# Optimization experiments

Hardware: AMD Instinct MI355X
Metric: run time of the kernel (lower is better)

## Reference

```python
import jax, jax.numpy as jnp
import numpy as np

B, T, V, D, DH, H = 4, 512, 32000, 768, 768, 4  # batch, seq, vocab, dim_in, dim_out(per-head & ffn), heads


def layer_norm(x, g, b, eps=1e-5):
    m = jnp.mean(x, axis=-1, keepdims=True)
    v = jnp.mean((x - m) ** 2, axis=-1, keepdims=True)
    return (x - m) * jax.lax.rsqrt(v + eps) * g + b


def setup_inputs() -> dict:
    key = jax.random.key(0)
    ks = jax.random.split(key, 20)
    s = 0.02
    f = lambda k, shp: (jax.random.normal(k, shp, jnp.float32) * s)
    return {
        "x": jax.random.randint(ks[0], (B, T), 0, V),
        "attention_mask": jax.random.randint(ks[1], (B, 1, T), 0, 2).astype(bool),
        "token_embed": f(ks[2], (V, D)),
        "segment_embed": f(ks[3], (V, D)),
        "ln_embed_g": jnp.ones((D,), jnp.float32), "ln_embed_b": jnp.zeros((D,), jnp.float32),
        "Wq": f(ks[4], (H, D, DH)), "bq": f(ks[5], (H, DH)),
        "Wk": f(ks[6], (H, D, DH)), "bk": f(ks[7], (H, DH)),
        "Wv": f(ks[8], (H, D, DH)), "bv": f(ks[9], (H, DH)),
        "Wo": f(ks[10], (H * DH, D)), "bo": f(ks[11], (D,)),
        "ln_attn_g": jnp.ones((D,), jnp.float32), "ln_attn_b": jnp.zeros((D,), jnp.float32),
        "W1": f(ks[12], (D, DH)), "b1": f(ks[13], (DH,)),
        "W2": f(ks[14], (DH, D)), "b2": f(ks[15], (D,)),
        "ln_enc_g": jnp.ones((D,), jnp.float32), "ln_enc_b": jnp.zeros((D,), jnp.float32),
        "Wproj": f(ks[16], (D, V)), "bproj": f(ks[17], (V,)),
        "Wcls": f(ks[18], (D, 2)), "bcls": f(ks[19], (2,)),
    }


def reference(x, attention_mask, token_embed, segment_embed, ln_embed_g, ln_embed_b,
              Wq, bq, Wk, bk, Wv, bv, Wo, bo, ln_attn_g, ln_attn_b,
              W1, b1, W2, b2, ln_enc_g, ln_enc_b, Wproj, bproj, Wcls, bcls):
    Bsz, Tlen = x.shape
    dim = token_embed.shape[1]
    # JointEmbedding: segment tensor is 0 for first half, 1 afterwards
    seg = jnp.zeros_like(x).at[:, Tlen // 2 + 1:].set(1)
    # positional encoding (faithful to source: exponent is 2*j/dim per column j,
    # sin on even columns, cos on odd columns, applied to pos/10000**exp)
    d = 2.0 * jnp.arange(dim, dtype=jnp.float32) / dim            # [D]
    p = jnp.arange(Tlen, dtype=jnp.float32)[:, None] / (10000.0 ** d)  # [T, D]
    pe = jnp.where(jnp.arange(dim) % 2 == 0, jnp.sin(p), jnp.cos(p))   # [T, D]
    emb = token_embed[x] + segment_embed[seg] + pe[None]          # [B, T, D]
    emb = layer_norm(emb, ln_embed_g, ln_embed_b)

    # Multi-head attention (vectorized over the per-head Python loop)
    Q = jnp.einsum('btd,hde->bhte', emb, Wq) + bq[None, :, None, :]
    K = jnp.einsum('btd,hde->bhte', emb, Wk) + bk[None, :, None, :]
    Vh = jnp.einsum('btd,hde->bhte', emb, Wv) + bv[None, :, None, :]
    # NOTE: source scales by seq_len**-0.5 (Q.size(1)), not head_dim**-0.5
    scores = jnp.einsum('bhte,bhse->bhts', Q, K) * (float(Tlen) ** -0.5)
    # NOTE: source masked_fill_'s with value 1e-9 (not -inf) before softmax
    scores = jnp.where(attention_mask[:, None, :, :], 1e-9, scores)
    attn = jax.nn.softmax(scores, axis=-1)
    ctx = jnp.einsum('bhts,bhse->bhte', attn, Vh)                 # [B, H, T, DH]
    cat = ctx.transpose(0, 2, 1, 3).reshape(Bsz, Tlen, -1)        # head concat order
    attn_out = layer_norm(cat @ Wo + bo, ln_attn_g, ln_attn_b)

    # FFN (no residual in source; dropout is identity at inference)
    h = jax.nn.gelu(attn_out @ W1 + b1, approximate=False)
    enc = layer_norm(h @ W2 + b2, ln_enc_g, ln_enc_b)

    token_pred = enc @ Wproj + bproj                              # [B, T, V]
    logits = jax.nn.log_softmax(token_pred, axis=-1)
    cls_out = enc[:, 0, :] @ Wcls + bcls                          # [B, 2]
    return logits, cls_out
```

## Files before the change

kernel.cpp:

```cpp
#include <hip/hip_runtime.h>
#include <hip/hip_bf16.h>
#include <stdint.h>

#define B_ 4
#define T_ 512
#define V_ 32000
#define D_ 768
#define DH_ 768
#define H_ 4
#define R_ 2048

typedef unsigned short u16;
typedef __attribute__((ext_vector_type(4))) float f32x4;
typedef __attribute__((ext_vector_type(8))) short s16x8;
typedef __attribute__((ext_vector_type(8))) unsigned short u16x8;
typedef __attribute__((address_space(3))) char* lds_cp;
typedef const __attribute__((address_space(1))) char* gl_cp;

__device__ __forceinline__ float bf2f(u16 u){
  union { float f; unsigned int i; } w; w.i = ((unsigned int)u) << 16; return w.f;
}
__device__ __forceinline__ u16 f2bf(float f){
  union { float f; unsigned int i; } w; w.f = f;
  unsigned int r = w.i + 0x7fffu + ((w.i >> 16) & 1u);
  return (u16)(r >> 16);
}

__device__ __forceinline__ float block_sum(float v, float* red){
  #pragma unroll
  for (int o = 32; o; o >>= 1) v += __shfl_down(v, o);
  __syncthreads();
  if ((threadIdx.x & 63) == 0) red[threadIdx.x >> 6] = v;
  __syncthreads();
  return red[0] + red[1] + red[2] + red[3];
}
__device__ __forceinline__ float block_max(float v, float* red){
  #pragma unroll
  for (int o = 32; o; o >>= 1) v = fmaxf(v, __shfl_down(v, o));
  __syncthreads();
  if ((threadIdx.x & 63) == 0) red[threadIdx.x >> 6] = v;
  __syncthreads();
  return fmaxf(fmaxf(red[0], red[1]), fmaxf(red[2], red[3]));
}

__global__ void mask_convert(const void* __restrict__ mraw, int* __restrict__ mout){
  __shared__ int isbyte;
  if (threadIdx.x == 0) isbyte = 0;
  __syncthreads();
  const unsigned char* by = (const unsigned char*)mraw;
  int f = 0;
  for (int i = threadIdx.x; i < 2048; i += 256)
    if ((i & 3) && by[i]) f = 1;
  if (f) atomicOr(&isbyte, 1);
  __syncthreads();
  if (isbyte){
    for (int i = threadIdx.x; i < 2048; i += 256) mout[i] = by[i] ? 1 : 0;
  } else {
    const int* mi = (const int*)mraw;
    for (int i = threadIdx.x; i < 2048; i += 256) mout[i] = mi[i] ? 1 : 0;
  }
}

__global__ __launch_bounds__(256)
void transpose_all(const float* __restrict__ Wq, const float* __restrict__ Wk,
                   const float* __restrict__ Wv, const float* __restrict__ Wo,
                   const float* __restrict__ W1, const float* __restrict__ W2,
                   u16* __restrict__ wqT, u16* __restrict__ wkT,
                   u16* __restrict__ wvT, u16* __restrict__ woT,
                   u16* __restrict__ w1T, u16* __restrict__ w2T){
  __shared__ u16 tile[32][33];
  int z = blockIdx.z;
  const float* in; u16* out; int out_ld = 768;
  if (z < 4)      { in = Wq + (long)z * 589824;        out = wqT + (long)z * 589824; }
  else if (z < 8) { int k = z - 4;  in = Wk + (long)k * 589824; out = wkT + (long)k * 589824; }
  else if (z < 12){ int k = z - 8;  in = Wv + (long)k * 589824; out = wvT + (long)k * 589824; }
  else if (z < 16){ int k = z - 12; in = Wo + (long)k * 589824; out = woT + (long)k * 768; out_ld = 3072; }
  else if (z == 16){ in = W1; out = w1T; }
  else             { in = W2; out = w2T; }
  int c0 = blockIdx.x * 32, r0 = blockIdx.y * 32;
  int tx = threadIdx.x & 31, ty = threadIdx.x >> 5;
  #pragma unroll
  for (int i = 0; i < 32; i += 8)
    tile[ty + i][tx] = f2bf(in[(long)(r0 + ty + i) * 768 + (c0 + tx)]);
  __syncthreads();
  #pragma unroll
  for (int i = 0; i < 32; i += 8)
    out[(long)(c0 + ty + i) * out_ld + (r0 + tx)] = tile[tx][ty + i];
}

__global__ __launch_bounds__(256)
void transpose_f2b(const float* __restrict__ in, u16* __restrict__ out, int R, int C){
  __shared__ u16 tile[32][33];
  int c0 = blockIdx.x * 32, r0 = blockIdx.y * 32;
  int tx = threadIdx.x & 31, ty = threadIdx.x >> 5;
  #pragma unroll
  for (int i = 0; i < 32; i += 8)
    tile[ty + i][tx] = f2bf(in[(long)(r0 + ty + i) * C + (c0 + tx)]);
  __syncthreads();
  #pragma unroll
  for (int i = 0; i < 32; i += 8)
    out[(long)(c0 + ty + i) * R + (r0 + tx)] = tile[tx][ty + i];
}

__global__ __launch_bounds__(256)
void embed_ln(const int* __restrict__ x, const float* __restrict__ tok,
              const float* __restrict__ seg, const float* __restrict__ g,
              const float* __restrict__ bb, u16* __restrict__ emb){
  __shared__ float red[4];
  int r = blockIdx.x, t = r & 511;
  int tid = threadIdx.x;
  long trow = (long)x[r] * D_;
  long srow = (t > 256) ? (long)D_ : 0;
  float v[3];
  float s = 0.f;
  #pragma unroll
  for (int q = 0; q < 3; ++q){
    int j = tid + q * 256;
    float d = (2.0f * (float)j) * (1.0f / 768.0f);
    float p = (float)t * powf(10000.0f, -d);
    float pe = (j & 1) ? cosf(p) : sinf(p);
    v[q] = tok[trow + j] + seg[srow + j] + pe;
    s += v[q];
  }
  float mean = block_sum(s, red) * (1.0f / 768.0f);
  float vs = 0.f;
  #pragma unroll
  for (int q = 0; q < 3; ++q){ float dd = v[q] - mean; vs += dd * dd; }
  float var = block_sum(vs, red) * (1.0f / 768.0f);
  float inv = rsqrtf(var + 1e-5f);
  #pragma unroll
  for (int q = 0; q < 3; ++q){
    int j = tid + q * 256;
    emb[(long)r * D_ + j] = f2bf((v[q] - mean) * inv * g[j] + bb[j]);
  }
}

__global__ __launch_bounds__(256)
void ln_rows(const u16* __restrict__ in, const float* __restrict__ g,
             const float* __restrict__ bb, u16* __restrict__ out){
  __shared__ float red[4];
  long r = blockIdx.x;
  int tid = threadIdx.x;
  const u16* row = in + r * D_;
  float v[3];
  float s = 0.f;
  #pragma unroll
  for (int q = 0; q < 3; ++q){ v[q] = bf2f(row[tid + q * 256]); s += v[q]; }
  float mean = block_sum(s, red) * (1.0f / 768.0f);
  float vs = 0.f;
  #pragma unroll
  for (int q = 0; q < 3; ++q){ float dd = v[q] - mean; vs += dd * dd; }
  float var = block_sum(vs, red) * (1.0f / 768.0f);
  float inv = rsqrtf(var + 1e-5f);
  #pragma unroll
  for (int q = 0; q < 3; ++q){
    int j = tid + q * 256;
    out[r * D_ + j] = f2bf((v[q] - mean) * inv * g[j] + bb[j]);
  }
}

__global__ __launch_bounds__(256)
void attn_softmax(u16* __restrict__ S, const int* __restrict__ mask){
  __shared__ float red[4];
  int t = blockIdx.x, z = blockIdx.y, b = z >> 2;
  u16* row = S + (long)z * (T_ * T_) + (long)t * T_;
  int tid = threadIdx.x;
  int s0 = tid, s1 = tid + 256;
  float v0 = mask[b * T_ + s0] ? 1e-9f : bf2f(row[s0]);
  float v1 = mask[b * T_ + s1] ? 1e-9f : bf2f(row[s1]);
  float mx = block_max(fmaxf(v0, v1), red);
  float e0 = expf(v0 - mx), e1 = expf(v1 - mx);
  float l = block_sum(e0 + e1, red);
  float inv = 1.0f / l;
  row[s0] = f2bf(e0 * inv);
  row[s1] = f2bf(e1 * inv);
}

__global__ __launch_bounds__(256)
void lsm_b2f(const u16* __restrict__ pred, float* __restrict__ out){
  __shared__ float sm[256], sl[256];
  long r = blockIdx.x;
  const u16x8* rv = (const u16x8*)(pred + r * (long)V_);
  int tid = threadIdx.x;
  float m = -1e30f, l = 0.f;
  for (int c = tid; c < V_ / 8; c += 256){
    u16x8 v = rv[c];
    #pragma unroll
    for (int j = 0; j < 8; ++j){
      float x = bf2f(v[j]);
      if (x > m){ l = l * expf(m - x) + 1.0f; m = x; }
      else l += expf(x - m);
    }
  }
  sm[tid] = m; sl[tid] = l;
  __syncthreads();
  #pragma unroll
  for (int s = 128; s; s >>= 1){
    if (tid < s){
      float m2 = sm[tid + s], l2 = sl[tid + s];
      float M = fmaxf(sm[tid], m2);
      sl[tid] = sl[tid] * expf(sm[tid] - M) + l2 * expf(m2 - M);
      sm[tid] = M;
    }
    __syncthreads();
  }
  float lse = sm[0] + logf(sl[0]);
  f32x4* orow = (f32x4*)(out + r * (long)V_);
  for (int c = tid; c < V_ / 8; c += 256){
    u16x8 v = rv[c];
    f32x4 o0, o1;
    #pragma unroll
    for (int j = 0; j < 4; ++j){ o0[j] = bf2f(v[j]) - lse; o1[j] = bf2f(v[j + 4]) - lse; }
    orow[2 * c] = o0; orow[2 * c + 1] = o1;
  }
}

__global__ __launch_bounds__(256)
void log_softmax_rows(float* __restrict__ tp){
  __shared__ float sm[256], sl[256];
  long r = blockIdx.x;
  float* row = tp + r * (long)V_;
  f32x4* rv = (f32x4*)row;
  int tid = threadIdx.x;
  float m = -1e30f, l = 0.f;
  for (int c = tid; c < V_ / 4; c += 256){
    f32x4 v = rv[c];
    #pragma unroll
    for (int j = 0; j < 4; ++j){
      float x = v[j];
      if (x > m){ l = l * expf(m - x) + 1.0f; m = x; }
      else l += expf(x - m);
    }
  }
  sm[tid] = m; sl[tid] = l;
  __syncthreads();
  #pragma unroll
  for (int s = 128; s; s >>= 1){
    if (tid < s){
      float m2 = sm[tid + s], l2 = sl[tid + s];
      float M = fmaxf(sm[tid], m2);
      sl[tid] = sl[tid] * expf(sm[tid] - M) + l2 * expf(m2 - M);
      sm[tid] = M;
    }
    __syncthreads();
  }
  float lse = sm[0] + logf(sl[0]);
  for (int c = tid; c < V_ / 4; c += 256){
    f32x4 v = rv[c];
    #pragma unroll
    for (int j = 0; j < 4; ++j) v[j] -= lse;
    rv[c] = v;
  }
}

__global__ __launch_bounds__(256)
void cls_head(const u16* __restrict__ enc, const float* __restrict__ Wc,
              const float* __restrict__ bc, float* __restrict__ out){
  int w = threadIdx.x >> 6, lane = threadIdx.x & 63;
  const u16* e = enc + (long)w * (T_ * D_);
  float a0 = 0.f, a1 = 0.f;
  for (int k = lane; k < D_; k += 64){
    float ev = bf2f(e[k]);
    a0 += ev * Wc[k * 2 + 0];
    a1 += ev * Wc[k * 2 + 1];
  }
  #pragma unroll
  for (int o = 32; o; o >>= 1){ a0 += __shfl_down(a0, o); a1 += __shfl_down(a1, o); }
  if (lane == 0){
    out[(long)B_ * T_ * V_ + w * 2 + 0] = a0 + bc[0];
    out[(long)B_ * T_ * V_ + w * 2 + 1] = a1 + bc[1];
  }
}

template<int GELU, int F32OUT>
__global__ __launch_bounds__(256, 2)
void gemm_bt(const u16* __restrict__ A, const u16* __restrict__ Bt,
             const float* __restrict__ bias, void* __restrict__ Cv,
             int lda, int ldb,
             long sAzb, long sAzh, long sBzb, long sBzh, long sbz,
             long sCzb, long sCzh, long sCb, long sCr, long sCc,
             int zsh, float scale, int nt){
  extern __shared__ char smem[];
  u16* sA = (u16*)smem;
  u16* sB = sA + 2 * 128 * 64;
  int tid = threadIdx.x, lane = tid & 63, wid = tid >> 6;
  int wm = wid >> 1, wn = wid & 1;
  int lrow = lane & 15, lquad = lane >> 4;

  unsigned gx = gridDim.x, gy = gridDim.y;
  unsigned nwg = gx * gy * gridDim.z;
  unsigned id = blockIdx.x + gx * (blockIdx.y + gy * blockIdx.z);
  unsigned qq = nwg >> 3, rr = nwg & 7, xcd = id & 7, loc = id >> 3;
  unsigned nid = (xcd < rr ? xcd * (qq + 1) : rr * (qq + 1) + (xcd - rr) * qq) + loc;
  unsigned bx = nid % gx, tmpq = nid / gx;
  unsigned by = tmpq % gy, bz = tmpq / gy;

  int z = (int)bz, zb = z >> zsh, zh = z & ((1 << zsh) - 1);
  long bm = (long)bx * 128, bn = (long)by * 128;
  const u16* Az = A + zb * sAzb + zh * sAzh;
  const u16* Bz = Bt + zb * sBzb + zh * sBzh;

  f32x4 acc[4][4] = {};

  auto stage = [&](int buf, int kt){
    #pragma unroll
    for (int q = 0; q < 4; ++q){
      int seg = wid * 4 + q;
      int idx = seg * 64 + lane;
      int r = idx >> 3, c = idx & 7;
      int ksw = (c ^ (r & 7)) << 3;
      const u16* srcA = Az + (bm + r) * lda + kt * 64 + ksw;
      const u16* srcB = Bz + (bn + r) * ldb + kt * 64 + ksw;
      __builtin_amdgcn_global_load_lds((gl_cp)srcA,
          (lds_cp)((char*)(sA + buf * 8192) + seg * 1024), 16, 0, 0);
      __builtin_amdgcn_global_load_lds((gl_cp)srcB,
          (lds_cp)((char*)(sB + buf * 8192) + seg * 1024), 16, 0, 0);
    }
  };

  stage(0, 0);
  __syncthreads();
  int cur = 0;
  for (int t = 0; t < nt; ++t){
    if (t + 1 < nt) stage(cur ^ 1, t + 1);
    const u16* a0 = sA + cur * 8192;
    const u16* b0 = sB + cur * 8192;
    #pragma unroll
    for (int kk = 0; kk < 2; ++kk){
      int koff = (((kk * 4 + lquad) ^ (lrow & 7)) << 3);
      s16x8 af[4], bfv[4];
      #pragma unroll
      for (int m = 0; m < 4; ++m)
        af[m] = *(const s16x8*)(a0 + (wm * 64 + m * 16 + lrow) * 64 + koff);
      #pragma unroll
      for (int n = 0; n < 4; ++n)
        bfv[n] = *(const s16x8*)(b0 + (wn * 64 + n * 16 + lrow) * 64 + koff);
      #pragma unroll
      for (int m = 0; m < 4; ++m)
        #pragma unroll
        for (int n = 0; n < 4; ++n)
          acc[m][n] = __builtin_amdgcn_mfma_f32_16x16x32_bf16(af[m], bfv[n], acc[m][n], 0, 0, 0);
    }
    __syncthreads();
    cur ^= 1;
  }

  long czbase = zb * sCzb + zh * sCzh;
  #pragma unroll
  for (int n = 0; n < 4; ++n){
    long col = bn + wn * 64 + n * 16 + lrow;
    float bv = bias ? bias[zb * sbz + col] : 0.f;
    #pragma unroll
    for (int m = 0; m < 4; ++m){
      #pragma unroll
      for (int j = 0; j < 4; ++j){
        long row = bm + wm * 64 + m * 16 + lquad * 4 + j;
        float v = acc[m][n][j] * scale + bv;
        if (GELU) v = 0.5f * v * (1.0f + erff(v * 0.70710678118654752f));
        long ci = czbase + (row >> 9) * sCb + (row & 511) * sCr + col * sCc;
        if (F32OUT) ((float*)Cv)[ci] = v;
        else        ((u16*)Cv)[ci] = f2bf(v);
      }
    }
  }
}

template<int F32OUT>
__global__ __launch_bounds__(512, 2)
void gemm8p(const u16* __restrict__ A, const u16* __restrict__ Bt,
            const float* __restrict__ bias, void* __restrict__ Cv){
  __shared__ char smem[131072];
  const int tid = threadIdx.x, lane = tid & 63, wid = tid >> 6;
  const int wm = wid >> 2, wn = wid & 3;
  const int lrow = lane & 15, lquad = lane >> 4;

  unsigned id = blockIdx.x + 8u * blockIdx.y;
  unsigned wg = (id & 7u) * 125u + (id >> 3);
  const long bm = (long)(wg & 7u) * 256;
  const long bn = (long)(wg >> 3) * 256;
  const int NT = 24;

  f32x4 acc[8][4] = {};

  auto stage_half = [&](int k, int kind, int h){
    int slot = k & 3;
    int r = tid >> 2, c = tid & 3;
    int lc = c ^ ((r >> 1) & 3);
    const u16* src = (kind ? Bt + (bn + h * 128 + r) * 768
                           : A  + (bm + h * 128 + r) * 768) + k * 32 + lc * 8;
    char* dst = smem + slot * 32768 + kind * 16384 + h * 8192 + (wid * 64) * 16;
    __builtin_amdgcn_global_load_lds((gl_cp)src, (lds_cp)dst, 16, 0, 0);
  };

  #pragma unroll
  for (int k = 0; k < 3; ++k){
    stage_half(k, 0, 0); stage_half(k, 0, 1);
    stage_half(k, 1, 0); stage_half(k, 1, 1);
  }
  asm volatile("s_waitcnt vmcnt(8)" ::: "memory");
  __builtin_amdgcn_s_barrier();
  __builtin_amdgcn_sched_barrier(0);

  const int ksw = (lquad ^ ((lrow >> 1) & 3)) * 16;
  for (int k = 0; k < NT; ++k){
    const char* slot = smem + (k & 3) * 32768;
    const char* aBase = slot + wm * 8192;
    const char* bBase = slot + 16384 + (wn >> 1) * 8192 + ((wn & 1) * 64) * 64;
    s16x8 af[4], bfv[4];

    #pragma unroll
    for (int nf = 0; nf < 4; ++nf)
      bfv[nf] = *(const s16x8*)(bBase + (nf * 16 + lrow) * 64 + ksw);
    #pragma unroll
    for (int mf = 0; mf < 4; ++mf)
      af[mf] = *(const s16x8*)(aBase + (mf * 16 + lrow) * 64 + ksw);
    if (k + 3 < NT){ stage_half(k + 3, 0, 0); stage_half(k + 3, 0, 1); }
    __builtin_amdgcn_s_barrier();
    asm volatile("s_waitcnt lgkmcnt(0)" ::: "memory");
    __builtin_amdgcn_sched_barrier(0);
    __builtin_amdgcn_s_setprio(1);
    #pragma unroll
    for (int mf = 0; mf < 4; ++mf)
      #pragma unroll
      for (int nf = 0; nf < 4; ++nf)
        acc[mf][nf] = __builtin_amdgcn_mfma_f32_16x16x32_bf16(af[mf], bfv[nf], acc[mf][nf], 0, 0, 0);
    __builtin_amdgcn_s_setprio(0);
    __builtin_amdgcn_sched_barrier(0);
    __builtin_amdgcn_s_barrier();

    #pragma unroll
    for (int mf = 0; mf < 4; ++mf)
      af[mf] = *(const s16x8*)(aBase + ((mf + 4) * 16 + lrow) * 64 + ksw);
    if (k + 3 < NT){ stage_half(k + 3, 1, 0); stage_half(k + 3, 1, 1); }
    __builtin_amdgcn_s_barrier();
    asm volatile("s_waitcnt lgkmcnt(0)" ::: "memory");
    __builtin_amdgcn_sched_barrier(0);
    __builtin_amdgcn_s_setprio(1);
    #pragma unroll
    for (int mf = 0; mf < 4; ++mf)
      #pragma unroll
      for (int nf = 0; nf < 4; ++nf)
        acc[mf + 4][nf] = __builtin_amdgcn_mfma_f32_16x16x32_bf16(af[mf], bfv[nf], acc[mf + 4][nf], 0, 0, 0);
    __builtin_amdgcn_s_setprio(0);
    __builtin_amdgcn_sched_barrier(0);
    if (k <= NT - 4)      { asm volatile("s_waitcnt vmcnt(8)" ::: "memory"); }
    else if (k == NT - 3) { asm volatile("s_waitcnt vmcnt(4)" ::: "memory"); }
    else if (k == NT - 2) { asm volatile("s_waitcnt vmcnt(0)" ::: "memory"); }
    __builtin_amdgcn_s_barrier();
    __builtin_amdgcn_sched_barrier(0);
  }

  #pragma unroll
  for (int nf = 0; nf < 4; ++nf){
    long col = bn + wn * 64 + nf * 16 + lrow;
    float bv = bias[col];
    #pragma unroll
    for (int mf = 0; mf < 8; ++mf){
      #pragma unroll
      for (int j = 0; j < 4; ++j){
        long row = bm + wm * 128 + mf * 16 + lquad * 4 + j;
        float v = acc[mf][nf][j] + bv;
        if (F32OUT) ((float*)Cv)[row * (long)V_ + col] = v;
        else        ((u16*)Cv)[row * (long)V_ + col] = f2bf(v);
      }
    }
  }
}

extern "C" void kernel_launch(void* const* d_in, const int* in_sizes, int n_in,
                              void* d_out, int out_size, void* d_ws, size_t ws_size,
                              hipStream_t stream){
  const int*   x     = (const int*)d_in[0];
  const void*  amask = d_in[1];
  const float* tok = (const float*)d_in[2];
  const float* seg = (const float*)d_in[3];
  const float* lng = (const float*)d_in[4];
  const float* lnb = (const float*)d_in[5];
  const float* Wq  = (const float*)d_in[6];
  const float* bq  = (const float*)d_in[7];
  const float* Wk  = (const float*)d_in[8];
  const float* bk  = (const float*)d_in[9];
  const float* Wv  = (const float*)d_in[10];
  const float* bv  = (const float*)d_in[11];
  const float* Wo  = (const float*)d_in[12];
  const float* bo  = (const float*)d_in[13];
  const float* lag = (const float*)d_in[14];
  const float* lab = (const float*)d_in[15];
  const float* W1  = (const float*)d_in[16];
  const float* b1  = (const float*)d_in[17];
  const float* W2  = (const float*)d_in[18];
  const float* b2  = (const float*)d_in[19];
  const float* leg = (const float*)d_in[20];
  const float* leb = (const float*)d_in[21];
  const float* Wp  = (const float*)d_in[22];
  const float* bp  = (const float*)d_in[23];
  const float* Wc  = (const float*)d_in[24];
  const float* bc  = (const float*)d_in[25];
  float* out = (float*)d_out;
  char* ws = (char*)d_ws;

  size_t off = 0;
  auto alloc = [&](size_t bytes){ size_t o = off; off += (bytes + 255) & ~(size_t)255; return o; };
  size_t o_mask = alloc(2048 * 4);
  size_t o_emb  = alloc((size_t)R_ * D_ * 2);
  size_t o_wqT  = alloc((size_t)H_ * D_ * DH_ * 2);
  size_t o_wkT  = alloc((size_t)H_ * D_ * DH_ * 2);
  size_t o_wvT  = alloc((size_t)H_ * D_ * DH_ * 2);
  size_t o_woT  = alloc((size_t)3072 * 768 * 2);
  size_t o_w1T  = alloc((size_t)768 * 768 * 2);
  size_t o_w2T  = alloc((size_t)768 * 768 * 2);
  size_t o_Q    = alloc((size_t)B_ * H_ * T_ * DH_ * 2);
  size_t o_K    = alloc((size_t)B_ * H_ * T_ * DH_ * 2);
  size_t o_VT   = alloc((size_t)B_ * H_ * DH_ * T_ * 2);
  size_t o_S    = alloc((size_t)B_ * H_ * T_ * T_ * 2);
  size_t o_cat  = alloc((size_t)R_ * 3072 * 2);
  size_t o_ap   = alloc((size_t)R_ * D_ * 2);
  size_t o_ao   = alloc((size_t)R_ * D_ * 2);
  size_t o_h1   = alloc((size_t)R_ * D_ * 2);
  size_t o_ep   = alloc((size_t)R_ * D_ * 2);
  size_t o_enc  = alloc((size_t)R_ * D_ * 2);
  size_t o_wpT  = o_Q;
  size_t off_base = off;
  size_t o_pred = alloc((size_t)R_ * V_ * 2);
  int bigws = (ws_size >= off);
  if (ws_size < off_base) return;

  int* maskI = (int*)(ws + o_mask);
  u16* emb  = (u16*)(ws + o_emb);
  u16* wqT  = (u16*)(ws + o_wqT);
  u16* wkT  = (u16*)(ws + o_wkT);
  u16* wvT  = (u16*)(ws + o_wvT);
  u16* woT  = (u16*)(ws + o_woT);
  u16* w1T  = (u16*)(ws + o_w1T);
  u16* w2T  = (u16*)(ws + o_w2T);
  u16* Qb   = (u16*)(ws + o_Q);
  u16* Kb   = (u16*)(ws + o_K);
  u16* VTb  = (u16*)(ws + o_VT);
  u16* Sb   = (u16*)(ws + o_S);
  u16* catb = (u16*)(ws + o_cat);
  u16* apb  = (u16*)(ws + o_ap);
  u16* aob  = (u16*)(ws + o_ao);
  u16* h1b  = (u16*)(ws + o_h1);
  u16* epb  = (u16*)(ws + o_ep);
  u16* encb = (u16*)(ws + o_enc);
  u16* wpT  = (u16*)(ws + o_wpT);
  u16* predb = (u16*)(ws + o_pred);

  const long sQK_zb = (long)H_ * T_ * DH_;
  const long sQK_zh = (long)T_ * DH_;

  mask_convert<<<1, 256, 0, stream>>>(amask, maskI);
  transpose_all<<<dim3(24, 24, 18), 256, 0, stream>>>(Wq, Wk, Wv, Wo, W1, W2,
      wqT, wkT, wvT, woT, w1T, w2T);
  embed_ln<<<R_, 256, 0, stream>>>(x, tok, seg, lng, lnb, emb);

  gemm_bt<0,0><<<dim3(16, 6, 4), 256, 65536, stream>>>(emb, wqT, bq, Qb,
      768, 768, 0, 0, (long)768 * 768, 0, 768,
      sQK_zh, 0, sQK_zb, 768, 1, 0, 1.0f, 12);
  gemm_bt<0,0><<<dim3(16, 6, 4), 256, 65536, stream>>>(emb, wkT, bk, Kb,
      768, 768, 0, 0, (long)768 * 768, 0, 768,
      sQK_zh, 0, sQK_zb, 768, 1, 0, 1.0f, 12);
  gemm_bt<0,0><<<dim3(16, 6, 4), 256, 65536, stream>>>(emb, wvT, bv, VTb,
      768, 768, 0, 0, (long)768 * 768, 0, 768,
      sQK_zh, 0, sQK_zb, 1, 512, 0, 1.0f, 12);

  gemm_bt<0,0><<<dim3(4, 4, 16), 256, 65536, stream>>>(Qb, Kb, nullptr, Sb,
      768, 768, sQK_zb, sQK_zh, sQK_zb, sQK_zh, 0,
      (long)H_ * T_ * T_, (long)T_ * T_, 0, 512, 1, 2, 0.044194173824159216f, 12);

  attn_softmax<<<dim3(512, 16), 256, 0, stream>>>(Sb, maskI);

  gemm_bt<0,0><<<dim3(4, 6, 16), 256, 65536, stream>>>(Sb, VTb, nullptr, catb,
      512, 512, (long)H_ * T_ * T_, (long)T_ * T_, sQK_zb, sQK_zh, 0,
      (long)T_ * 3072, 768, 0, 3072, 1, 2, 1.0f, 8);

  gemm_bt<0,0><<<dim3(16, 6, 1), 256, 65536, stream>>>(catb, woT, bo, apb,
      3072, 3072, 0, 0, 0, 0, 0,
      0, 0, (long)512 * 768, 768, 1, 0, 1.0f, 48);
  ln_rows<<<R_, 256, 0, stream>>>(apb, lag, lab, aob);

  gemm_bt<1,0><<<dim3(16, 6, 1), 256, 65536, stream>>>(aob, w1T, b1, h1b,
      768, 768, 0, 0, 0, 0, 0,
      0, 0, (long)512 * 768, 768, 1, 0, 1.0f, 12);
  gemm_bt<0,0><<<dim3(16, 6, 1), 256, 65536, stream>>>(h1b, w2T, b2, epb,
      768, 768, 0, 0, 0, 0, 0,
      0, 0, (long)512 * 768, 768, 1, 0, 1.0f, 12);
  ln_rows<<<R_, 256, 0, stream>>>(epb, leg, leb, encb);

  transpose_f2b<<<dim3(1000, 24, 1), 256, 0, stream>>>(Wp, wpT, 768, 32000);

  if (bigws){
    gemm8p<0><<<dim3(8, 125), 512, 0, stream>>>(encb, wpT, bp, predb);
    lsm_b2f<<<R_, 256, 0, stream>>>(predb, out);
  } else {
    gemm8p<1><<<dim3(8, 125), 512, 0, stream>>>(encb, wpT, bp, out);
    log_softmax_rows<<<R_, 256, 0, stream>>>(out);
  }
  cls_head<<<1, 256, 0, stream>>>(encb, Wc, bc, out);

  (void)in_sizes; (void)n_in; (void)out_size;
}
```

Before: 502.4 us.

## Software-pipeline LDS fragment loads across k-steps in vocab projection GEMM

Restructures the main loop of the vocab projection GEMM so the next k-tile's A/B fragments are read from LDS while the second half of the current tile's MFMAs runs. All four global-to-LDS stages for tile k+3 are issued at the top of the iteration, and three of the four barriers per iteration are removed. This aims to hide LDS read latency behind MFMA work and cut synchronisation overhead. In exchange it raises register pressure from the double-buffered fragments, and the vmcnt accounting has to line up exactly with the new issue order.

```diff
diff --git a/kernel.cpp b/kernel.cpp
--- a/kernel.cpp
+++ b/kernel.cpp
@@ -391,63 +391,82 @@
     char* dst = smem + slot * 32768 + kind * 16384 + h * 8192 + (wid * 64) * 16;
     __builtin_amdgcn_global_load_lds((gl_cp)src, (lds_cp)dst, 16, 0, 0);
   };
+  const int ksw = (lquad ^ ((lrow >> 1) & 3)) * 16;
+  auto aBaseOf = [&](int k){ return smem + (k & 3) * 32768 + wm * 8192; };
+  auto bBaseOf = [&](int k){
+    return smem + (k & 3) * 32768 + 16384 + (wn >> 1) * 8192 + ((wn & 1) * 64) * 64;
+  };
 
   #pragma unroll
   for (int k = 0; k < 3; ++k){
     stage_half(k, 0, 0); stage_half(k, 0, 1);
     stage_half(k, 1, 0); stage_half(k, 1, 1);
   }
-  asm volatile("s_waitcnt vmcnt(8)" ::: "memory");
+  asm volatile("s_waitcnt vmcnt(4)" ::: "memory");
   __builtin_amdgcn_s_barrier();
   __builtin_amdgcn_sched_barrier(0);
 
-  const int ksw = (lquad ^ ((lrow >> 1) & 3)) * 16;
+  s16x8 af0[4], bfv[4];
+  {
+    const char* aB = aBaseOf(0); const char* bB = bBaseOf(0);
+    #pragma unroll
+    for (int nf = 0; nf < 4; ++nf)
+      bfv[nf] = *(const s16x8*)(bB + (nf * 16 + lrow) * 64 + ksw);
+    #pragma unroll
+    for (int mf = 0; mf < 4; ++mf)
+      af0[mf] = *(const s16x8*)(aB + (mf * 16 + lrow) * 64 + ksw);
+  }
+  asm volatile("s_waitcnt lgkmcnt(0)" ::: "memory");
+  __builtin_amdgcn_sched_barrier(0);
+
   for (int k = 0; k < NT; ++k){
-    const char* slot = smem + (k & 3) * 32768;
-    const char* aBase = slot + wm * 8192;
-    const char* bBase = slot + 16384 + (wn >> 1) * 8192 + ((wn & 1) * 64) * 64;
-    s16x8 af[4], bfv[4];
-
-    #pragma unroll
-    for (int nf = 0; nf < 4; ++nf)
-      bfv[nf] = *(const s16x8*)(bBase + (nf * 16 + lrow) * 64 + ksw);
+    const char* aB = aBaseOf(k);
+    if (k + 3 < NT){
+      stage_half(k + 3, 0, 0); stage_half(k + 3, 0, 1);
+      stage_half(k + 3, 1, 0); stage_half(k + 3, 1, 1);
+    }
+    s16x8 af1[4];
     #pragma unroll
     for (int mf = 0; mf < 4; ++mf)
-      af[mf] = *(const s16x8*)(aBase + (mf * 16 + lrow) * 64 + ksw);
-    if (k + 3 < NT){ stage_half(k + 3, 0, 0); stage_half(k + 3, 0, 1); }
-    __builtin_amdgcn_s_barrier();
+      af1[mf] = *(const s16x8*)(aB + ((mf + 4) * 16 + lrow) * 64 + ksw);
+    __builtin_amdgcn_sched_barrier(0);
+    __builtin_amdgcn_s_setprio(1);
+    #pragma unroll
+    for (int mf = 0; mf < 4; ++mf)
+      #pragma unroll
+      for (int nf = 0; nf < 4; ++nf)
+        acc[mf][nf] = __builtin_amdgcn_mfma_f32_16x16x32_bf16(af0[mf], bfv[nf], acc[mf][nf], 0, 0, 0);
+    __builtin_amdgcn_s_setprio(0);
+    __builtin_amdgcn_sched_barrier(0);
     asm volatile("s_waitcnt lgkmcnt(0)" ::: "memory");
     __builtin_amdgcn_sched_barrier(0);
+    s16x8 afn[4], bfn[4];
+    if (k + 1 < NT){
+      const char* aN = aBaseOf(k + 1); const char* bN = bBaseOf(k + 1);
+      #pragma unroll
+      for (int nf = 0; nf < 4; ++nf)
+        bfn[nf] = *(const s16x8*)(bN + (nf * 16 + lrow) * 64 + ksw);
+      #pragma unroll
+      for (int mf = 0; mf < 4; ++mf)
+        afn[mf] = *(const s16x8*)(aN + (mf * 16 + lrow) * 64 + ksw);
+    }
+    __builtin_amdgcn_sched_barrier(0);
     __builtin_amdgcn_s_setprio(1);
     #pragma unroll
     for (int mf = 0; mf < 4; ++mf)
       #pragma unroll
       for (int nf = 0; nf < 4; ++nf)
-        acc[mf][nf] = __builtin_amdgcn_mfma_f32_16x16x32_bf16(af[mf], bfv[nf], acc[mf][nf], 0, 0, 0);
+        acc[mf + 4][nf] = __builtin_amdgcn_mfma_f32_16x16x32_bf16(af1[mf], bfv[nf], acc[mf + 4][nf], 0, 0, 0);
     __builtin_amdgcn_s_setprio(0);
     __builtin_amdgcn_sched_barrier(0);
-    __builtin_amdgcn_s_barrier();
-
-    #pragma unroll
-    for (int mf = 0; mf < 4; ++mf)
-      af[mf] = *(const s16x8*)(aBase + ((mf + 4) * 16 + lrow) * 64 + ksw);
-    if (k + 3 < NT){ stage_half(k + 3, 1, 0); stage_half(k + 3, 1, 1); }
-    __builtin_amdgcn_s_barrier();
     asm volatile("s_waitcnt lgkmcnt(0)" ::: "memory");
     __builtin_amdgcn_sched_barrier(0);
-    __builtin_amdgcn_s_setprio(1);
-    #pragma unroll
-    for (int mf = 0; mf < 4; ++mf)
-      #pragma unroll
-      for (int nf = 0; nf < 4; ++nf)
-        acc[mf + 4][nf] = __builtin_amdgcn_mfma_f32_16x16x32_bf16(af[mf], bfv[nf], acc[mf + 4][nf], 0, 0, 0);
-    __builtin_amdgcn_s_setprio(0);
-    __builtin_amdgcn_sched_barrier(0);
-    if (k <= NT - 4)      { asm volatile("s_waitcnt vmcnt(8)" ::: "memory"); }
-    else if (k == NT - 3) { asm volatile("s_waitcnt vmcnt(4)" ::: "memory"); }
-    else if (k == NT - 2) { asm volatile("s_waitcnt vmcnt(0)" ::: "memory"); }
+    if (k <= NT - 4)      { asm volatile("s_waitcnt vmcnt(4)" ::: "memory"); }
+    else if (k == NT - 3) { asm volatile("s_waitcnt vmcnt(0)" ::: "memory"); }
     __builtin_amdgcn_s_barrier();
     __builtin_amdgcn_sched_barrier(0);
+    #pragma unroll
+    for (int i = 0; i < 4; ++i){ af0[i] = afn[i]; bfv[i] = bfn[i]; }
   }
 
   #pragma unroll
```

Measured after the change: 498.7 us. About the same (-0.7%).
